# Performance work log

Measured on AMD Instinct MI355X. Metric: run time of the kernel, lower is better.

Reference implementation:

```python
import jax, jax.numpy as jnp
import numpy as np

N_NODES = 10000
N_EDGES = 160000
S1, V1 = 64, 32   # node irreps: 64x0e + 32x1e
S2, V2 = 16, 8    # edge irreps: 16x0e + 8x1e
N_GATE = V1       # one sigmoid gate scalar per output vector channel
S_OUT = S1 + N_GATE  # 96 scalar TP outputs (features + gates)
FAN_IN = 1280.0   # = S1*S2 + V1*V2 = S1*V2 + V1*S2 + V1*V2 (same for both outputs)
BN_EPS = 1e-5

# Levi-Civita tensor for the 1x1->1 (cross product) CG path
_lc = np.zeros((3, 3, 3), dtype=np.float32)
_lc[0, 1, 2] = _lc[1, 2, 0] = _lc[2, 0, 1] = 1.0
_lc[0, 2, 1] = _lc[2, 1, 0] = _lc[1, 0, 2] = -1.0
LC = jnp.asarray(_lc)


def setup_inputs() -> dict:
    key = jax.random.key(0)
    ks = jax.random.split(key, 8)
    return {
        'x': jax.random.normal(ks[0], (N_NODES, S1 + 3 * V1), dtype=jnp.float32),
        'edge_attr': jax.random.normal(ks[1], (N_EDGES, S2 + 3 * V2), dtype=jnp.float32),
        'W_ss': jax.random.normal(ks[2], (S1, S2, S_OUT), dtype=jnp.float32),
        'W_vv_s': jax.random.normal(ks[3], (V1, V2, S_OUT), dtype=jnp.float32),
        'W_sv': jax.random.normal(ks[4], (S1, V2, V1), dtype=jnp.float32),
        'W_vs': jax.random.normal(ks[5], (V1, S2, V1), dtype=jnp.float32),
        'W_vv_v': jax.random.normal(ks[6], (V1, V2, V1), dtype=jnp.float32),
        'bn_w_s': jnp.ones((S1,), dtype=jnp.float32),
        'bn_b_s': jnp.zeros((S1,), dtype=jnp.float32),
        'bn_w_v': jnp.ones((V1,), dtype=jnp.float32),
        'edge_index': jax.random.randint(ks[7], (2, N_EDGES), 0, N_NODES, dtype=jnp.int64),
    }


def reference(x, edge_attr, W_ss, W_vv_s, W_sv, W_vs, W_vv_v, bn_w_s, bn_b_s, bn_w_v, edge_index):
    i = edge_index[0]
    n = x.shape[0]

    # gather node features per edge; split into scalar / vector irreps
    xs = x[i]                                   # [E, 160]
    s1 = xs[:, :S1]                             # [E, 64]
    v1 = xs[:, S1:].reshape(-1, V1, 3)          # [E, 32, 3]
    s2 = edge_attr[:, :S2]                      # [E, 16]
    v2 = edge_attr[:, S2:].reshape(-1, V2, 3)   # [E, 8, 3]

    inv = 1.0 / np.sqrt(FAN_IN).astype(np.float32)

    # fully-connected equivariant tensor product (Clebsch-Gordan paths)
    s_out = (jnp.einsum('ea,eb,abc->ec', s1, s2, W_ss, optimize=True)
             + jnp.einsum('eam,ebm,abc->ec', v1, v2, W_vv_s, optimize=True) / np.sqrt(3.0)) * inv
    v_out = (jnp.einsum('ea,ebm,abc->ecm', s1, v2, W_sv, optimize=True)
             + jnp.einsum('eam,eb,abc->ecm', v1, s2, W_vs, optimize=True)
             + jnp.einsum('eam,ebn,mnp,abc->ecp', v1, v2, LC, W_vv_v, optimize=True) / np.sqrt(2.0)) * inv

    # swish gate: swish on feature scalars, sigmoid gates multiply vectors
    feat = jax.nn.silu(s_out[:, :S1])           # [E, 64]
    gate = jax.nn.sigmoid(s_out[:, S1:])        # [E, 32]
    v_g = v_out * gate[:, :, None]              # [E, 32, 3]

    # scatter-reduce (sum) back to nodes
    s_n = jax.ops.segment_sum(feat, i, num_segments=n)                             # [N, 64]
    v_n = jax.ops.segment_sum(v_g.reshape(-1, 3 * V1), i, num_segments=n).reshape(n, V1, 3)

    # equivariant batchnorm: standard BN on scalars, norm-only BN on vectors
    mu = s_n.mean(axis=0)
    var = jnp.mean((s_n - mu) ** 2, axis=0)
    s_bn = (s_n - mu) / jnp.sqrt(var + BN_EPS) * bn_w_s + bn_b_s
    vnorm = jnp.mean(jnp.sum(v_n ** 2, axis=-1), axis=0) / 3.0                     # [32]
    v_bn = v_n / jnp.sqrt(vnorm + BN_EPS)[None, :, None] * bn_w_v[None, :, None]

    # residual
    return jnp.concatenate([s_bn, v_bn.reshape(n, 3 * V1)], axis=-1) + x
```

## Files before the change

kernel.cpp:

```cpp
#include <hip/hip_runtime.h>
#include <hip/hip_bf16.h>


#define NNODES 10000
#define NEDGES 160000
#define EB 128
#define FSTRD 66

typedef unsigned short u16;
typedef unsigned int u32;
typedef short short8 __attribute__((ext_vector_type(8)));
typedef float f32x4 __attribute__((ext_vector_type(4)));

__device__ __forceinline__ u16 f2b(float f) {
  union { float f; u32 i; } v; v.f = f;
  u32 r = v.i + 0x7FFFu + ((v.i >> 16) & 1u);
  return (u16)(r >> 16);
}
__device__ __forceinline__ float lo_f(u32 d) {
  union { u32 i; float f; } v; v.i = d << 16; return v.f;
}
__device__ __forceinline__ float hi_f(u32 d) {
  union { u32 i; float f; } v; v.i = d & 0xFFFF0000u; return v.f;
}
__device__ __forceinline__ u32 pk2(float lo, float hi) {
  return __builtin_amdgcn_perm(__float_as_uint(hi), __float_as_uint(lo), 0x07060302u);
}
union frag_u { u32 w[4]; short8 s; };

#define INVF  0.02795084971874737f
#define INV3  0.5773502691896258f
#define INV2  0.7071067811865476f

__global__ void prep_kernel(const float* __restrict__ W_ss, const float* __restrict__ W_vv_s,
                            const float* __restrict__ W_sv, const float* __restrict__ W_vs,
                            const float* __restrict__ W_vv_v,
                            u32* __restrict__ WSd, u32* __restrict__ WVd,
                            float* __restrict__ zbase, int zcount) {
  int t = blockIdx.x * 256 + threadIdx.x;
  if (t < zcount) zbase[t] = 0.f;
  if (t < 61440) {
    int d = t;
    int nt = d / 10240, r = d - nt * 10240;
    int kt = r >> 8, l = (r & 255) >> 2, jp = r & 3;
    int n = nt * 16 + (l & 15);
    int k0 = kt * 32 + ((l >> 4) << 3) + jp * 2;
    float f0, f1;
    f0 = (k0     < 1024) ? W_ss[k0 * 96 + n] * INVF       : W_vv_s[(k0 - 1024) * 96 + n] * (INVF * INV3);
    f1 = (k0 + 1 < 1024) ? W_ss[(k0 + 1) * 96 + n] * INVF : W_vv_s[(k0 - 1023) * 96 + n] * (INVF * INV3);
    WSd[d] = (u32)f2b(f0) | ((u32)f2b(f1) << 16);
  } else if (t < 81920) {
    int d = t - 61440;
    int nt = d / 10240, r = d - nt * 10240;
    int kt = r >> 8, l = (r & 255) >> 2, jp = r & 3;
    int n = nt * 16 + (l & 15);
    int k0 = kt * 32 + ((l >> 4) << 3) + jp * 2;
    float f[2];
#pragma unroll
    for (int jj = 0; jj < 2; jj++) {
      int k = k0 + jj;
      if (k < 512)       f[jj] = W_sv[k * 32 + n] * INVF;
      else if (k < 1024) f[jj] = W_vs[(k - 512) * 32 + n] * INVF;
      else               f[jj] = W_vv_v[(k - 1024) * 32 + n] * (INVF * INV2);
    }
    WVd[d] = (u32)f2b(f[0]) | ((u32)f2b(f[1]) << 16);
  }
}

__global__ void count_kernel(const int* __restrict__ eidx, int* __restrict__ cnt) {
  int t = blockIdx.x * 256 + threadIdx.x;
  if (t < NEDGES) atomicAdd(&cnt[eidx[t]], 1);
}

__global__ void scan_kernel(const int* __restrict__ cnt, int* __restrict__ off,
                            int* __restrict__ cursor) {
  __shared__ int part[1024];
  int t = threadIdx.x;
  int local[10]; int s = 0;
  if (t < 1000) {
#pragma unroll
    for (int i = 0; i < 10; i++) { local[i] = cnt[t * 10 + i]; s += local[i]; }
  }
  part[t] = s; __syncthreads();
  for (int d = 1; d < 1024; d <<= 1) {
    int v = (t >= d) ? part[t - d] : 0; __syncthreads();
    part[t] += v; __syncthreads();
  }
  if (t < 1000) {
    int ex = (t == 0) ? 0 : part[t - 1];
#pragma unroll
    for (int i = 0; i < 10; i++) { off[t * 10 + i] = ex; cursor[t * 10 + i] = ex; ex += local[i]; }
  }
  if (t == 0) off[10000] = NEDGES;
}

__global__ void fill_kernel(const int* __restrict__ eidx, int* __restrict__ cursor,
                            int* __restrict__ elist) {
  int t = blockIdx.x * 256 + threadIdx.x;
  if (t < NEDGES) {
    int slot = atomicAdd(&cursor[eidx[t]], 1);
    elist[slot] = t;
  }
}

__global__ __launch_bounds__(256, 2) void edge_kernel(
    const float* __restrict__ x, const float* __restrict__ ea,
    const int* __restrict__ eidx,
    const u16* __restrict__ WSp, const u16* __restrict__ WVp,
    float* __restrict__ s_n, float* __restrict__ v_n,
    u16* __restrict__ ms16, u16* __restrict__ mv16, int use_msg) {
  __shared__ int idxL[EB];
  __shared__ u32 fTd[200 * FSTRD];
  const int tid = threadIdx.x;
  const int eb = blockIdx.x * EB;

  if (tid < EB) idxL[tid] = eidx[eb + tid];
  __syncthreads();
#pragma unroll 1
  for (int t = tid; t < 64 * 200; t += 256) {
    int ep = t / 200, j = t - ep * 200;
    float vlo, vhi;
    if (j < 160) {
      vlo = x[(size_t)idxL[ep] * 160 + j];
      vhi = x[(size_t)idxL[ep + 64] * 160 + j];
    } else {
      vlo = ea[(size_t)(eb + ep) * 40 + (j - 160)];
      vhi = ea[(size_t)(eb + ep + 64) * 40 + (j - 160)];
    }
    fTd[j * FSTRD + ep] = (u32)f2b(vlo) | ((u32)f2b(vhi) << 16);
  }
  __syncthreads();

  const int wv = tid >> 6, lane = tid & 63;
  const int ln = lane & 15, quad = lane >> 4;
  const int ep = wv * 16 + ln;
  const int qh = quad >> 1, bb = (quad & 1) * 8;

  float s2l[8], s2h[8], v2l[24], v2h[24];
#pragma unroll
  for (int i = 0; i < 8; i++) {
    u32 d = fTd[(160 + bb + i) * FSTRD + ep];
    s2l[i] = lo_f(d); s2h[i] = hi_f(d);
  }
#pragma unroll
  for (int i = 0; i < 24; i++) {
    u32 d = fTd[(176 + i) * FSTRD + ep];
    v2l[i] = lo_f(d); v2h[i] = hi_f(d);
  }

  const u16* WS_l = WSp + (size_t)lane * 8;
  const u16* WV_l = WVp + (size_t)lane * 8;

#define LOAD_BS(B, ktv) { _Pragma("unroll") \
  for (int nt = 0; nt < 6; nt++) B[nt].s = *(const short8*)(WS_l + (size_t)(ktv) * 512 + nt * 20480); }
#define LOAD_BV(C, ktv) { _Pragma("unroll") \
  for (int nt = 0; nt < 2; nt++) C[nt].s = *(const short8*)(WV_l + (size_t)(ktv) * 512 + nt * 20480); }
#define MFMA_S(Al, Ah, B) { _Pragma("unroll") \
  for (int nt = 0; nt < 6; nt++) { \
    aS[0][nt] = __builtin_amdgcn_mfma_f32_16x16x32_bf16(Al.s, B[nt].s, aS[0][nt], 0, 0, 0); \
    aS[1][nt] = __builtin_amdgcn_mfma_f32_16x16x32_bf16(Ah.s, B[nt].s, aS[1][nt], 0, 0, 0); } }
#define MFMA_V(Al, Ah, C, p) { \
    aV[0][p][0] = __builtin_amdgcn_mfma_f32_16x16x32_bf16(Al.s, C[0].s, aV[0][p][0], 0, 0, 0); \
    aV[0][p][1] = __builtin_amdgcn_mfma_f32_16x16x32_bf16(Al.s, C[1].s, aV[0][p][1], 0, 0, 0); \
    aV[1][p][0] = __builtin_amdgcn_mfma_f32_16x16x32_bf16(Ah.s, C[0].s, aV[1][p][0], 0, 0, 0); \
    aV[1][p][1] = __builtin_amdgcn_mfma_f32_16x16x32_bf16(Ah.s, C[1].s, aV[1][p][1], 0, 0, 0); }

  f32x4 aS[2][6];
#pragma unroll
  for (int t = 0; t < 2; t++)
#pragma unroll
    for (int i = 0; i < 6; i++) aS[t][i] = (f32x4){0.f, 0.f, 0.f, 0.f};

  frag_u B0[6], B1[6];
  LOAD_BS(B0, 0);

#pragma unroll 1
  for (int c = 0; c < 16; c++) {
    int kt = 2 * c;
    u32 dA = fTd[(2 * kt + qh) * FSTRD + ep];
    u32 dB = fTd[(2 * kt + 2 + qh) * FSTRD + ep];
    LOAD_BS(B1, kt + 1);
    {
      frag_u Al, Ah;
      float slo = lo_f(dA), shi = hi_f(dA);
#pragma unroll
      for (int jp = 0; jp < 4; jp++) {
        Al.w[jp] = pk2(slo * s2l[2 * jp], slo * s2l[2 * jp + 1]);
        Ah.w[jp] = pk2(shi * s2h[2 * jp], shi * s2h[2 * jp + 1]);
      }
      MFMA_S(Al, Ah, B0);
    }
    LOAD_BS(B0, kt + 2);
    {
      frag_u Al, Ah;
      float slo = lo_f(dB), shi = hi_f(dB);
#pragma unroll
      for (int jp = 0; jp < 4; jp++) {
        Al.w[jp] = pk2(slo * s2l[2 * jp], slo * s2l[2 * jp + 1]);
        Ah.w[jp] = pk2(shi * s2h[2 * jp], shi * s2h[2 * jp + 1]);
      }
      MFMA_S(Al, Ah, B1);
    }
  }
#pragma unroll 1
  for (int c = 0; c < 4; c++) {
    int kt = 32 + 2 * c;
    int r0 = (64 + (4 * (kt - 32) + quad) * 3) * FSTRD + ep;
    int r1 = r0 + 12 * FSTRD;
    u32 d0 = fTd[r0], d1 = fTd[r0 + FSTRD], d2 = fTd[r0 + 2 * FSTRD];
    u32 e0 = fTd[r1], e1 = fTd[r1 + FSTRD], e2 = fTd[r1 + 2 * FSTRD];
    LOAD_BS(B1, kt + 1);
    {
      frag_u Al, Ah;
      float x0 = lo_f(d0), x1 = lo_f(d1), x2 = lo_f(d2);
      float y0 = hi_f(d0), y1 = hi_f(d1), y2 = hi_f(d2);
#pragma unroll
      for (int jp = 0; jp < 4; jp++) {
        int j0 = 6 * jp, j1 = 6 * jp + 3;
        Al.w[jp] = pk2(x0*v2l[j0] + x1*v2l[j0+1] + x2*v2l[j0+2],
                       x0*v2l[j1] + x1*v2l[j1+1] + x2*v2l[j1+2]);
        Ah.w[jp] = pk2(y0*v2h[j0] + y1*v2h[j0+1] + y2*v2h[j0+2],
                       y0*v2h[j1] + y1*v2h[j1+1] + y2*v2h[j1+2]);
      }
      MFMA_S(Al, Ah, B0);
    }
    LOAD_BS(B0, kt + 2);
    {
      frag_u Al, Ah;
      float x0 = lo_f(e0), x1 = lo_f(e1), x2 = lo_f(e2);
      float y0 = hi_f(e0), y1 = hi_f(e1), y2 = hi_f(e2);
#pragma unroll
      for (int jp = 0; jp < 4; jp++) {
        int j0 = 6 * jp, j1 = 6 * jp + 3;
        Al.w[jp] = pk2(x0*v2l[j0] + x1*v2l[j0+1] + x2*v2l[j0+2],
                       x0*v2l[j1] + x1*v2l[j1+1] + x2*v2l[j1+2]);
        Ah.w[jp] = pk2(y0*v2h[j0] + y1*v2h[j0+1] + y2*v2h[j0+2],
                       y0*v2h[j1] + y1*v2h[j1+1] + y2*v2h[j1+2]);
      }
      MFMA_S(Al, Ah, B1);
    }
  }

  frag_u C0[2], C1[2];
  LOAD_BV(C0, 32);

  float gateR[16];
#pragma unroll
  for (int t = 0; t < 2; t++) {
#pragma unroll
    for (int r = 0; r < 4; r++) {
      int er = wv * 16 + quad * 4 + r + t * 64;
      int nid = idxL[er];
#pragma unroll
      for (int nt = 0; nt < 6; nt++) {
        float v = aS[t][nt][r];
        float sg = 1.f / (1.f + __expf(-v));
        if (nt < 4) {
          if (use_msg) ms16[(size_t)(eb + er) * 64 + nt * 16 + ln] = f2b(v * sg);
          else         atomicAdd(&s_n[nid * 64 + nt * 16 + ln], v * sg);
        } else gateR[t * 8 + (nt - 4) * 4 + r] = sg;
      }
    }
  }

  f32x4 aV[2][3][2];
#pragma unroll
  for (int t = 0; t < 2; t++)
#pragma unroll
    for (int p = 0; p < 3; p++)
#pragma unroll
      for (int nt = 0; nt < 2; nt++) aV[t][p][nt] = (f32x4){0.f, 0.f, 0.f, 0.f};

#pragma unroll 1
  for (int c = 0; c < 4; c++) {
    int kt = 32 + 2 * c;
    int r0 = (64 + (4 * (kt - 32) + quad) * 3) * FSTRD + ep;
    int r1 = r0 + 12 * FSTRD;
    u32 d0 = fTd[r0], d1 = fTd[r0 + FSTRD], d2 = fTd[r0 + 2 * FSTRD];
    u32 e0 = fTd[r1], e1 = fTd[r1 + FSTRD], e2 = fTd[r1 + 2 * FSTRD];
    LOAD_BV(C1, kt + 1);
    {
      float wl[3] = { lo_f(d0), lo_f(d1), lo_f(d2) };
      float wh[3] = { hi_f(d0), hi_f(d1), hi_f(d2) };
#pragma unroll
      for (int p = 0; p < 3; p++) {
        const int p1 = (p + 1) % 3, p2 = (p + 2) % 3;
        frag_u Al, Ah;
#pragma unroll
        for (int jp = 0; jp < 4; jp++) {
          int j0 = 6 * jp, j1 = 6 * jp + 3;
          Al.w[jp] = pk2(wl[p1]*v2l[j0+p2] - wl[p2]*v2l[j0+p1],
                         wl[p1]*v2l[j1+p2] - wl[p2]*v2l[j1+p1]);
          Ah.w[jp] = pk2(wh[p1]*v2h[j0+p2] - wh[p2]*v2h[j0+p1],
                         wh[p1]*v2h[j1+p2] - wh[p2]*v2h[j1+p1]);
        }
        MFMA_V(Al, Ah, C0, p);
      }
    }
    LOAD_BV(C0, (c < 3) ? (kt + 2) : 0);
    {
      float wl[3] = { lo_f(e0), lo_f(e1), lo_f(e2) };
      float wh[3] = { hi_f(e0), hi_f(e1), hi_f(e2) };
#pragma unroll
      for (int p = 0; p < 3; p++) {
        const int p1 = (p + 1) % 3, p2 = (p + 2) % 3;
        frag_u Al, Ah;
#pragma unroll
        for (int jp = 0; jp < 4; jp++) {
          int j0 = 6 * jp, j1 = 6 * jp + 3;
          Al.w[jp] = pk2(wl[p1]*v2l[j0+p2] - wl[p2]*v2l[j0+p1],
                         wl[p1]*v2l[j1+p2] - wl[p2]*v2l[j1+p1]);
          Ah.w[jp] = pk2(wh[p1]*v2h[j0+p2] - wh[p2]*v2h[j0+p1],
                         wh[p1]*v2h[j1+p2] - wh[p2]*v2h[j1+p1]);
        }
        MFMA_V(Al, Ah, C1, p);
      }
    }
  }
#pragma unroll 1
  for (int c = 0; c < 8; c++) {
    int kt = 2 * c;
    u32 dA = fTd[(4 * kt + quad) * FSTRD + ep];
    u32 dB = fTd[(4 * kt + 4 + quad) * FSTRD + ep];
    LOAD_BV(C1, kt + 1);
    {
      float slo = lo_f(dA), shi = hi_f(dA);
#pragma unroll
      for (int p = 0; p < 3; p++) {
        frag_u Al, Ah;
#pragma unroll
        for (int jp = 0; jp < 4; jp++) {
          Al.w[jp] = pk2(slo * v2l[(2*jp)*3 + p], slo * v2l[(2*jp+1)*3 + p]);
          Ah.w[jp] = pk2(shi * v2h[(2*jp)*3 + p], shi * v2h[(2*jp+1)*3 + p]);
        }
        MFMA_V(Al, Ah, C0, p);
      }
    }
    LOAD_BV(C0, kt + 2);
    {
      float slo = lo_f(dB), shi = hi_f(dB);
#pragma unroll
      for (int p = 0; p < 3; p++) {
        frag_u Al, Ah;
#pragma unroll
        for (int jp = 0; jp < 4; jp++) {
          Al.w[jp] = pk2(slo * v2l[(2*jp)*3 + p], slo * v2l[(2*jp+1)*3 + p]);
          Ah.w[jp] = pk2(shi * v2h[(2*jp)*3 + p], shi * v2h[(2*jp+1)*3 + p]);
        }
        MFMA_V(Al, Ah, C1, p);
      }
    }
  }
#pragma unroll 1
  for (int c = 0; c < 8; c++) {
    int kt = 16 + 2 * c;
    int r0 = (64 + (2 * (kt - 16) + qh) * 3) * FSTRD + ep;
    int r1 = r0 + 6 * FSTRD;
    u32 d0 = fTd[r0], d1 = fTd[r0 + FSTRD], d2 = fTd[r0 + 2 * FSTRD];
    u32 e0 = fTd[r1], e1 = fTd[r1 + FSTRD], e2 = fTd[r1 + 2 * FSTRD];
    LOAD_BV(C1, kt + 1);
    {
      float vl[3] = { lo_f(d0), lo_f(d1), lo_f(d2) };
      float vh[3] = { hi_f(d0), hi_f(d1), hi_f(d2) };
#pragma unroll
      for (int p = 0; p < 3; p++) {
        frag_u Al, Ah;
#pragma unroll
        for (int jp = 0; jp < 4; jp++) {
          Al.w[jp] = pk2(vl[p] * s2l[2*jp], vl[p] * s2l[2*jp+1]);
          Ah.w[jp] = pk2(vh[p] * s2h[2*jp], vh[p] * s2h[2*jp+1]);
        }
        MFMA_V(Al, Ah, C0, p);
      }
    }
    LOAD_BV(C0, (c < 7) ? (kt + 2) : 0);
    {
      float vl[3] = { lo_f(e0), lo_f(e1), lo_f(e2) };
      float vh[3] = { hi_f(e0), hi_f(e1), hi_f(e2) };
#pragma unroll
      for (int p = 0; p < 3; p++) {
        frag_u Al, Ah;
#pragma unroll
        for (int jp = 0; jp < 4; jp++) {
          Al.w[jp] = pk2(vl[p] * s2l[2*jp], vl[p] * s2l[2*jp+1]);
          Ah.w[jp] = pk2(vh[p] * s2h[2*jp], vh[p] * s2h[2*jp+1]);
        }
        MFMA_V(Al, Ah, C1, p);
      }
    }
  }

#pragma unroll
  for (int t = 0; t < 2; t++) {
#pragma unroll
    for (int r = 0; r < 4; r++) {
      int er = wv * 16 + quad * 4 + r + t * 64;
      int nid = idxL[er];
#pragma unroll
      for (int nt = 0; nt < 2; nt++) {
        int c = nt * 16 + ln;
        float g = gateR[t * 8 + nt * 4 + r];
#pragma unroll
        for (int p = 0; p < 3; p++) {
          float val = aV[t][p][nt][r] * g;
          if (use_msg) mv16[(size_t)p * 5120000 + (size_t)(eb + er) * 32 + c] = f2b(val);
          else         atomicAdd(&v_n[nid * 96 + c * 3 + p], val);
        }
      }
    }
  }
}

__global__ __launch_bounds__(256) void gather_kernel(
    const int* __restrict__ off, const int* __restrict__ elist,
    const u32* __restrict__ msd, const u32* __restrict__ mvd,
    float* __restrict__ s_n, float* __restrict__ v_n) {
  int tid = threadIdx.x;
  int n = blockIdx.x * 4 + (tid >> 6);
  int lane = tid & 63;
  int beg = off[n], end = off[n + 1];
  float a0 = 0.f, a1 = 0.f, b0 = 0.f, b1 = 0.f, c0 = 0.f, c1 = 0.f;
  int pp = (lane < 48) ? 0 : 1, dd = lane & 15;
#pragma unroll 1
  for (int k = beg; k < end; k++) {
    int e = elist[k];
    if (lane < 32) { u32 w = msd[(size_t)e * 32 + lane]; a0 += lo_f(w); a1 += hi_f(w); }
    else           { u32 w = mvd[(size_t)pp * 2560000 + (size_t)e * 16 + dd]; b0 += lo_f(w); b1 += hi_f(w); }
    if (lane < 16) { u32 w = mvd[(size_t)2 * 2560000 + (size_t)e * 16 + lane]; c0 += lo_f(w); c1 += hi_f(w); }
  }
  if (lane < 32) {
    s_n[n * 64 + 2 * lane] = a0; s_n[n * 64 + 2 * lane + 1] = a1;
  } else {
    v_n[n * 96 + (2 * dd) * 3 + pp] = b0; v_n[n * 96 + (2 * dd + 1) * 3 + pp] = b1;
  }
  if (lane < 16) {
    v_n[n * 96 + (2 * lane) * 3 + 2] = c0; v_n[n * 96 + (2 * lane + 1) * 3 + 2] = c1;
  }
}

__global__ void stats_kernel(const float* __restrict__ s_n, const float* __restrict__ v_n,
                             float* __restrict__ stats) {
  int b = blockIdx.x, tid = threadIdx.x;
  int r0 = b * 50;
  int c = tid & 63, rg = tid >> 6;
  float s = 0.f, sq = 0.f;
  for (int r = r0 + rg; r < r0 + 50; r += 4) {
    float v = s_n[r * 64 + c];
    s += v; sq += v * v;
  }
  atomicAdd(&stats[c], s);
  atomicAdd(&stats[64 + c], sq);
  int c2 = tid & 31, rg2 = tid >> 5;
  float vn = 0.f;
  for (int r = r0 + rg2; r < r0 + 50; r += 8) {
    const float* vp = &v_n[r * 96 + c2 * 3];
    vn += vp[0] * vp[0] + vp[1] * vp[1] + vp[2] * vp[2];
  }
  atomicAdd(&stats[128 + c2], vn);
}

__global__ void finalize_kernel(const float* __restrict__ s_n, const float* __restrict__ v_n,
                                const float* __restrict__ stats,
                                const float* __restrict__ x,
                                const float* __restrict__ bw_s, const float* __restrict__ bb_s,
                                const float* __restrict__ bw_v,
                                float* __restrict__ out) {
  int t = blockIdx.x * 256 + threadIdx.x;
  if (t >= NNODES * 160) return;
  int n = t / 160, j = t - n * 160;
  float xv = x[t];
  float r;
  if (j < 64) {
    float mu  = stats[j] * (1.f / NNODES);
    float var = stats[64 + j] * (1.f / NNODES) - mu * mu;
    var = fmaxf(var, 0.f);
    float v = s_n[n * 64 + j];
    r = (v - mu) * rsqrtf(var + 1e-5f) * bw_s[j] + bb_s[j];
  } else {
    int qq = j - 64;
    int c = qq / 3;
    float vn = stats[128 + c] * (1.f / (3.f * NNODES));
    float v = v_n[n * 96 + qq];
    r = v * rsqrtf(vn + 1e-5f) * bw_v[c];
  }
  out[t] = r + xv;
}

extern "C" void kernel_launch(void* const* d_in, const int* in_sizes, int n_in,
                              void* d_out, int out_size, void* d_ws, size_t ws_size,
                              hipStream_t stream) {
  const float* x      = (const float*)d_in[0];
  const float* ea     = (const float*)d_in[1];
  const float* W_ss   = (const float*)d_in[2];
  const float* W_vv_s = (const float*)d_in[3];
  const float* W_sv   = (const float*)d_in[4];
  const float* W_vs   = (const float*)d_in[5];
  const float* W_vv_v = (const float*)d_in[6];
  const float* bw_s   = (const float*)d_in[7];
  const float* bb_s   = (const float*)d_in[8];
  const float* bw_v   = (const float*)d_in[9];
  const int* eidx     = (const int*)d_in[10];
  float* out = (float*)d_out;

  float* ws    = (float*)d_ws;
  u16* WSp     = (u16*)d_ws;
  u16* WVp     = WSp + 122880;
  float* s_n   = ws + 81920;
  float* v_n   = s_n + 640000;
  float* stats = v_n + 960000;
  int* cnt     = (int*)(ws + 1682080);
  int* off     = (int*)(ws + 1692080);
  int* cursor  = (int*)(ws + 1702084);
  int* elist   = (int*)(ws + 1712084);
  u32* msd     = (u32*)(ws + 1872084);
  u32* mvd     = msd + 5120000;

  int use_msg = (ws_size >= 58688336ULL) ? 1 : 0;

  if (use_msg)
    prep_kernel<<<6251, 256, 0, stream>>>(W_ss, W_vv_s, W_sv, W_vs, W_vv_v,
                                          (u32*)WSp, (u32*)WVp, stats, 10160);
  else
    prep_kernel<<<6251, 256, 0, stream>>>(W_ss, W_vv_s, W_sv, W_vs, W_vv_v,
                                          (u32*)WSp, (u32*)WVp, s_n, 1600160);
  if (use_msg) {
    count_kernel<<<625, 256, 0, stream>>>(eidx, cnt);
    scan_kernel<<<1, 1024, 0, stream>>>(cnt, off, cursor);
    fill_kernel<<<625, 256, 0, stream>>>(eidx, cursor, elist);
  }
  edge_kernel<<<NEDGES / EB, 256, 0, stream>>>(x, ea, eidx, WSp, WVp, s_n, v_n,
                                               (u16*)msd, (u16*)mvd, use_msg);
  if (use_msg)
    gather_kernel<<<2500, 256, 0, stream>>>(off, elist, msd, mvd, s_n, v_n);
  stats_kernel<<<200, 256, 0, stream>>>(s_n, v_n, stats);
  finalize_kernel<<<(NNODES * 160 + 255) / 256, 256, 0, stream>>>(
      s_n, v_n, stats, x, bw_s, bb_s, bw_v, out);
}
```

Before: 421.2 us.

## Interleave per-edge messages into one contiguous row and batch edge-list loads

Per-edge scalar and vector messages are now stored in a single 160-element bf16 row per edge, in node-output order, rather than in separate scalar and per-component vector planes. The gather kernel reads each edge's message as one contiguous 320-byte span and loads edge indices 64 at a time, broadcasting them with shuffles instead of one load per iteration. The LDS stride is also changed from 66 to 65, presumably to reduce bank conflicts. The edge kernel's vector stores become strided within a row, which may coalesce less well.

```diff
diff --git a/kernel.cpp b/kernel.cpp
--- a/kernel.cpp
+++ b/kernel.cpp
@@ -5,7 +5,7 @@
 #define NNODES 10000
 #define NEDGES 160000
 #define EB 128
-#define FSTRD 66
+#define FSTRD 65
 
 typedef unsigned short u16;
 typedef unsigned int u32;
@@ -108,7 +108,7 @@
     const int* __restrict__ eidx,
     const u16* __restrict__ WSp, const u16* __restrict__ WVp,
     float* __restrict__ s_n, float* __restrict__ v_n,
-    u16* __restrict__ ms16, u16* __restrict__ mv16, int use_msg) {
+    u16* __restrict__ msg16, int use_msg) {
   __shared__ int idxL[EB];
   __shared__ u32 fTd[200 * FSTRD];
   const int tid = threadIdx.x;
@@ -256,7 +256,7 @@
         float v = aS[t][nt][r];
         float sg = 1.f / (1.f + __expf(-v));
         if (nt < 4) {
-          if (use_msg) ms16[(size_t)(eb + er) * 64 + nt * 16 + ln] = f2b(v * sg);
+          if (use_msg) msg16[(size_t)(eb + er) * 160 + nt * 16 + ln] = f2b(v * sg);
           else         atomicAdd(&s_n[nid * 64 + nt * 16 + ln], v * sg);
         } else gateR[t * 8 + (nt - 4) * 4 + r] = sg;
       }
@@ -403,7 +403,7 @@
 #pragma unroll
         for (int p = 0; p < 3; p++) {
           float val = aV[t][p][nt][r] * g;
-          if (use_msg) mv16[(size_t)p * 5120000 + (size_t)(eb + er) * 32 + c] = f2b(val);
+          if (use_msg) msg16[(size_t)(eb + er) * 160 + 64 + c * 3 + p] = f2b(val);
           else         atomicAdd(&v_n[nid * 96 + c * 3 + p], val);
         }
       }
@@ -413,28 +413,37 @@
 
 __global__ __launch_bounds__(256) void gather_kernel(
     const int* __restrict__ off, const int* __restrict__ elist,
-    const u32* __restrict__ msd, const u32* __restrict__ mvd,
-    float* __restrict__ s_n, float* __restrict__ v_n) {
+    const u32* __restrict__ msg, float* __restrict__ s_n, float* __restrict__ v_n) {
   int tid = threadIdx.x;
   int n = blockIdx.x * 4 + (tid >> 6);
   int lane = tid & 63;
   int beg = off[n], end = off[n + 1];
-  float a0 = 0.f, a1 = 0.f, b0 = 0.f, b1 = 0.f, c0 = 0.f, c1 = 0.f;
-  int pp = (lane < 48) ? 0 : 1, dd = lane & 15;
-#pragma unroll 1
-  for (int k = beg; k < end; k++) {
-    int e = elist[k];
-    if (lane < 32) { u32 w = msd[(size_t)e * 32 + lane]; a0 += lo_f(w); a1 += hi_f(w); }
-    else           { u32 w = mvd[(size_t)pp * 2560000 + (size_t)e * 16 + dd]; b0 += lo_f(w); b1 += hi_f(w); }
-    if (lane < 16) { u32 w = mvd[(size_t)2 * 2560000 + (size_t)e * 16 + lane]; c0 += lo_f(w); c1 += hi_f(w); }
-  }
-  if (lane < 32) {
-    s_n[n * 64 + 2 * lane] = a0; s_n[n * 64 + 2 * lane + 1] = a1;
+  float a0 = 0.f, a1 = 0.f, b0 = 0.f, b1 = 0.f;
+#pragma unroll 1
+  for (int k0 = beg; k0 < end; k0 += 64) {
+    int m = end - k0; if (m > 64) m = 64;
+    int myE = (lane < m) ? elist[k0 + lane] : 0;
+#pragma unroll 2
+    for (int k = 0; k < m; k++) {
+      int e = __shfl(myE, k);
+      u32 w0 = msg[(size_t)e * 80 + lane];
+      a0 += lo_f(w0); a1 += hi_f(w0);
+      if (lane < 16) {
+        u32 w1 = msg[(size_t)e * 80 + 64 + lane];
+        b0 += lo_f(w1); b1 += hi_f(w1);
+      }
+    }
+  }
+  int ch = 2 * lane;
+  if (ch < 64) {
+    s_n[n * 64 + ch] = a0; s_n[n * 64 + ch + 1] = a1;
   } else {
-    v_n[n * 96 + (2 * dd) * 3 + pp] = b0; v_n[n * 96 + (2 * dd + 1) * 3 + pp] = b1;
+    int q = ch - 64;
+    v_n[n * 96 + q] = a0; v_n[n * 96 + q + 1] = a1;
   }
   if (lane < 16) {
-    v_n[n * 96 + (2 * lane) * 3 + 2] = c0; v_n[n * 96 + (2 * lane + 1) * 3 + 2] = c1;
+    int q = 64 + 2 * lane;
+    v_n[n * 96 + q] = b0; v_n[n * 96 + q + 1] = b1;
   }
 }
 
@@ -512,26 +521,24 @@
   int* off     = (int*)(ws + 1692080);
   int* cursor  = (int*)(ws + 1702084);
   int* elist   = (int*)(ws + 1712084);
-  u32* msd     = (u32*)(ws + 1872084);
-  u32* mvd     = msd + 5120000;
+  u32* msg     = (u32*)(ws + 1872084);
 
   int use_msg = (ws_size >= 58688336ULL) ? 1 : 0;
 
-  if (use_msg)
+  if (use_msg) {
     prep_kernel<<<6251, 256, 0, stream>>>(W_ss, W_vv_s, W_sv, W_vs, W_vv_v,
                                           (u32*)WSp, (u32*)WVp, stats, 10160);
-  else
-    prep_kernel<<<6251, 256, 0, stream>>>(W_ss, W_vv_s, W_sv, W_vs, W_vv_v,
-                                          (u32*)WSp, (u32*)WVp, s_n, 1600160);
-  if (use_msg) {
     count_kernel<<<625, 256, 0, stream>>>(eidx, cnt);
     scan_kernel<<<1, 1024, 0, stream>>>(cnt, off, cursor);
     fill_kernel<<<625, 256, 0, stream>>>(eidx, cursor, elist);
+  } else {
+    prep_kernel<<<6251, 256, 0, stream>>>(W_ss, W_vv_s, W_sv, W_vs, W_vv_v,
+                                          (u32*)WSp, (u32*)WVp, s_n, 1600160);
   }
   edge_kernel<<<NEDGES / EB, 256, 0, stream>>>(x, ea, eidx, WSp, WVp, s_n, v_n,
-                                               (u16*)msd, (u16*)mvd, use_msg);
+                                               (u16*)msg, use_msg);
   if (use_msg)
-    gather_kernel<<<2500, 256, 0, stream>>>(off, elist, msd, mvd, s_n, v_n);
+    gather_kernel<<<2500, 256, 0, stream>>>(off, elist, msg, s_n, v_n);
   stats_kernel<<<200, 256, 0, stream>>>(s_n, v_n, stats);
   finalize_kernel<<<(NNODES * 160 + 255) / 256, 256, 0, stream>>>(
       s_n, v_n, stats, x, bw_s, bb_s, bw_v, out);
```

After: 390.9 us. 1.08x faster.
